# Kernel optimization log

Measured on AMD Instinct MI355X. Metric: run time of the kernel, lower is better.

Reference implementation:

```python
import jax, jax.numpy as jnp
import numpy as np

N, N_EMB, HEAD, N_SEG = 8192, 256, 64, 128  # 128 molecules x 64 atoms


def setup_inputs() -> dict:
    key = jax.random.key(0)
    k0, k1, k2, k3, k4, k5 = jax.random.split(key, 6)
    X = jax.random.normal(k0, (N, N_EMB), dtype=jnp.float32)
    Z = jax.random.normal(k1, (N, 3), dtype=jnp.float32) * 3.0  # coordinates (Angstrom-ish)
    # CSR segment boundaries: 128 equal molecules of 64 atoms
    ptr = jnp.arange(N_SEG + 1, dtype=jnp.int32) * (N // N_SEG)
    scale = 1.0 / np.sqrt(N_EMB)
    Wk = jax.random.normal(k2, (HEAD, N_EMB), dtype=jnp.float32) * scale
    Wq = jax.random.normal(k3, (HEAD, N_EMB), dtype=jnp.float32) * scale
    Wv = jax.random.normal(k4, (HEAD, N_EMB), dtype=jnp.float32) * scale
    # invr0 = (rand(1) + 0.5) / cutoff, cutoff = 4.0
    invr0 = (jax.random.uniform(k5, (1,), dtype=jnp.float32) + 0.5) / 4.0
    return {"X": X, "Z": Z, "Wk": Wk, "Wq": Wq, "Wv": Wv, "invr0": invr0, "ptr": ptr}


def reference(X, Z, Wk, Wq, Wv, invr0, ptr):
    head_size = Wk.shape[0]
    n = X.shape[0]
    K = X @ Wk.T  # [N, H]
    Q = X @ Wq.T  # [N, H]
    V = X @ Wv.T  # [N, H]
    wei = (Q @ K.T) * (head_size ** -0.5)  # [N, N]
    # block-diagonal mask from segment boundaries (== torch.block_diag of ones blocks)
    seg = jnp.searchsorted(ptr[1:], jnp.arange(n, dtype=ptr.dtype), side="right")
    mask = seg[:, None] == seg[None, :]
    wei = jnp.where(mask, wei, -jnp.inf)
    wei = jax.nn.softmax(wei, axis=-1)
    # Euclidean cdist via gram trick, safe sqrt (zero grad at d2<=0, like torch.cdist)
    z2 = jnp.sum(Z * Z, axis=-1)
    d2 = jnp.maximum(z2[:, None] + z2[None, :] - 2.0 * (Z @ Z.T), 0.0)
    dist = jnp.sqrt(jnp.where(d2 > 0, d2, 1.0)) * (d2 > 0)
    wei = wei * jnp.exp(-invr0[0] * dist)
    out = wei @ V  # [N, H]
    return out
```

## Files before the change

### kernel.cpp

```cpp
#include <hip/hip_runtime.h>

#define NATOMS 8192
#define EMB    256
#define HEAD   64
#define WP     264
#define PB     72

typedef _Float16 f16;
typedef f16   f16x8 __attribute__((ext_vector_type(8)));
typedef f16   f16x4 __attribute__((ext_vector_type(4)));
typedef float f32x4 __attribute__((ext_vector_type(4)));

__global__ __launch_bounds__(512) void fused_kernel(
    const float* __restrict__ X, const float* __restrict__ Z,
    const float* __restrict__ Wk, const float* __restrict__ Wq,
    const float* __restrict__ Wv, const float* __restrict__ invr0p,
    float* __restrict__ out)
{
  union __align__(16) SMem {
    struct {
      f16 Xs[64 * WP];
      f16 Ws[192 * WP];
    } a;
    struct {
      f16 Qb[32 * PB];
      f16 Kb[64 * PB];
      f16 Vt[64 * PB];
      f16 Pb[32 * PB];
      float2 part[4][32];
      float zx[64], zy[64], zz[64];
    } b;
  };
  __shared__ SMem sm;

  const int tid  = threadIdx.x;
  const int seg  = blockIdx.x >> 1;
  const int hf   = blockIdx.x & 1;
  const int base = seg * 64;

  const int wave = tid >> 6;
  const int lane = tid & 63;
  const int fr   = lane & 15;
  const int fq   = lane >> 4;
  const int mf0  = (wave >> 2) * 2;
  const int nf0  = (wave & 3) * 3;

  const float ir = invr0p[0];
  float zr0 = 0.f, zr1 = 0.f, zr2 = 0.f;
  if (tid < 64) {
    const float* zp = Z + (size_t)(base + tid) * 3;
    zr0 = zp[0]; zr1 = zp[1]; zr2 = zp[2];
  }

  float4 xv[8];
  #pragma unroll
  for (int i = 0; i < 8; ++i) {
    const int f = tid + i * 512;
    const int row = f >> 6, c4 = f & 63;
    xv[i] = *reinterpret_cast<const float4*>(
        X + (size_t)(base + row) * EMB + c4 * 4);
  }
  float4 wv1[12];
  #pragma unroll
  for (int i = 0; i < 12; ++i) {
    const int f = tid + i * 512;
    const int row = f >> 6, c4 = f & 63;
    const float* src = (row < 64) ? (Wq + (size_t)row * EMB)
                                  : (Wk + (size_t)(row - 64) * EMB);
    wv1[i] = *reinterpret_cast<const float4*>(src + c4 * 4);
  }
  #pragma unroll
  for (int i = 0; i < 8; ++i) {
    const int f = tid + i * 512;
    const int row = f >> 6, c4 = f & 63;
    f16x4 h = {(f16)xv[i].x, (f16)xv[i].y, (f16)xv[i].z, (f16)xv[i].w};
    *reinterpret_cast<f16x4*>(&sm.a.Xs[row * WP + c4 * 4]) = h;
  }
  float4 wv2[12];
  #pragma unroll
  for (int i = 0; i < 12; ++i) {
    const int f = tid + (12 + i) * 512;
    const int row = f >> 6, c4 = f & 63;
    const float* src = (row < 128) ? (Wk + (size_t)(row - 64) * EMB)
                                   : (Wv + (size_t)(row - 128) * EMB);
    wv2[i] = *reinterpret_cast<const float4*>(src + c4 * 4);
  }
  #pragma unroll
  for (int i = 0; i < 12; ++i) {
    const int f = tid + i * 512;
    const int row = f >> 6, c4 = f & 63;
    f16x4 h = {(f16)wv1[i].x, (f16)wv1[i].y, (f16)wv1[i].z, (f16)wv1[i].w};
    *reinterpret_cast<f16x4*>(&sm.a.Ws[row * WP + c4 * 4]) = h;
  }
  #pragma unroll
  for (int i = 0; i < 12; ++i) {
    const int f = tid + (12 + i) * 512;
    const int row = f >> 6, c4 = f & 63;
    f16x4 h = {(f16)wv2[i].x, (f16)wv2[i].y, (f16)wv2[i].z, (f16)wv2[i].w};
    *reinterpret_cast<f16x4*>(&sm.a.Ws[row * WP + c4 * 4]) = h;
  }
  __syncthreads();

  f32x4 acc[2][3];
  #pragma unroll
  for (int m = 0; m < 2; ++m)
    #pragma unroll
    for (int n = 0; n < 3; ++n) acc[m][n] = (f32x4){0.f, 0.f, 0.f, 0.f};

  #pragma unroll
  for (int c = 0; c < 4; ++c) {
    #pragma unroll
    for (int ks = 0; ks < 2; ++ks) {
      const int ko = c * 64 + ks * 32 + fq * 8;
      const f16x8 a0 = *reinterpret_cast<const f16x8*>(
          &sm.a.Xs[((mf0 + 0) * 16 + fr) * WP + ko]);
      const f16x8 a1 = *reinterpret_cast<const f16x8*>(
          &sm.a.Xs[((mf0 + 1) * 16 + fr) * WP + ko]);
      #pragma unroll
      for (int n = 0; n < 3; ++n) {
        const f16x8 b = *reinterpret_cast<const f16x8*>(
            &sm.a.Ws[((nf0 + n) * 16 + fr) * WP + ko]);
        acc[0][n] = __builtin_amdgcn_mfma_f32_16x16x32_f16(a0, b, acc[0][n], 0, 0, 0);
        acc[1][n] = __builtin_amdgcn_mfma_f32_16x16x32_f16(a1, b, acc[1][n], 0, 0, 0);
      }
    }
  }
  __syncthreads();

  #pragma unroll
  for (int m = 0; m < 2; ++m) {
    const int mf = mf0 + m;
    const int rr = mf * 16 + fq * 4;
    #pragma unroll
    for (int n = 0; n < 3; ++n) {
      const int nf  = nf0 + n;
      const int col = nf * 16 + fr;
      if (nf < 4) {
        if ((mf >> 1) == hf) {
          const int qr = rr & 31;
          #pragma unroll
          for (int j = 0; j < 4; ++j)
            sm.b.Qb[(qr + j) * PB + col] = (f16)(acc[m][n][j] * 0.125f);
        }
      } else if (nf < 8) {
        #pragma unroll
        for (int j = 0; j < 4; ++j)
          sm.b.Kb[(rr + j) * PB + (col - 64)] = (f16)acc[m][n][j];
      } else {
        f16x4 hv = {(f16)acc[m][n][0], (f16)acc[m][n][1],
                    (f16)acc[m][n][2], (f16)acc[m][n][3]};
        *reinterpret_cast<f16x4*>(&sm.b.Vt[(col - 128) * PB + rr]) = hv;
      }
    }
  }
  if (tid < 64) {
    sm.b.zx[tid] = zr0; sm.b.zy[tid] = zr1; sm.b.zz[tid] = zr2;
  }
  __syncthreads();

  const int kf = wave & 3;
  const int qf = wave >> 2;
  f32x4 s = (f32x4){0.f, 0.f, 0.f, 0.f};
  #pragma unroll
  for (int hs = 0; hs < 2; ++hs) {
    const int ho = hs * 32 + fq * 8;
    const f16x8 kfrag = *reinterpret_cast<const f16x8*>(
        &sm.b.Kb[(kf * 16 + fr) * PB + ho]);
    const f16x8 qfrag = *reinterpret_cast<const f16x8*>(
        &sm.b.Qb[(qf * 16 + fr) * PB + ho]);
    s = __builtin_amdgcn_mfma_f32_16x16x32_f16(kfrag, qfrag, s, 0, 0, 0);
  }

  float m16 = fmaxf(fmaxf(s[0], s[1]), fmaxf(s[2], s[3]));
  m16 = fmaxf(m16, __shfl_xor(m16, 16));
  m16 = fmaxf(m16, __shfl_xor(m16, 32));
  float e[4]; float s16 = 0.f;
  #pragma unroll
  for (int j = 0; j < 4; ++j) { e[j] = __expf(s[j] - m16); s16 += e[j]; }
  s16 += __shfl_xor(s16, 16);
  s16 += __shfl_xor(s16, 32);
  if (fq == 0) sm.b.part[kf][qf * 16 + fr] = make_float2(m16, s16);
  __syncthreads();

  const float2 p0 = sm.b.part[0][qf * 16 + fr];
  const float2 p1 = sm.b.part[1][qf * 16 + fr];
  const float2 p2 = sm.b.part[2][qf * 16 + fr];
  const float2 p3 = sm.b.part[3][qf * 16 + fr];
  const float mg = fmaxf(fmaxf(p0.x, p1.x), fmaxf(p2.x, p3.x));
  const float sum = p0.y * __expf(p0.x - mg) + p1.y * __expf(p1.x - mg)
                  + p2.y * __expf(p2.x - mg) + p3.y * __expf(p3.x - mg);
  const float myscale = __expf(m16 - mg) / sum;

  const int   ri = hf * 32 + qf * 16 + fr;
  const float rx = sm.b.zx[ri], ry = sm.b.zy[ri], rz = sm.b.zz[ri];
  f16x4 pv;
  #pragma unroll
  for (int j = 0; j < 4; ++j) {
    const int ka = kf * 16 + fq * 4 + j;
    const float dx = rx - sm.b.zx[ka];
    const float dy = ry - sm.b.zy[ka];
    const float dz = rz - sm.b.zz[ka];
    const float dist = sqrtf(dx * dx + dy * dy + dz * dz);
    pv[j] = (f16)(e[j] * myscale * __expf(-ir * dist));
  }
  *reinterpret_cast<f16x4*>(
      &sm.b.Pb[(qf * 16 + fr) * PB + kf * 16 + fq * 4]) = pv;
  __syncthreads();

  const int qf2 = wave & 1;
  const int hb  = wave >> 1;
  f32x4 o = (f32x4){0.f, 0.f, 0.f, 0.f};
  #pragma unroll
  for (int ks2 = 0; ks2 < 2; ++ks2) {
    const int ko2 = ks2 * 32 + fq * 8;
    const f16x8 pf = *reinterpret_cast<const f16x8*>(
        &sm.b.Pb[(qf2 * 16 + fr) * PB + ko2]);
    const f16x8 vf = *reinterpret_cast<const f16x8*>(
        &sm.b.Vt[(hb * 16 + fr) * PB + ko2]);
    o = __builtin_amdgcn_mfma_f32_16x16x32_f16(pf, vf, o, 0, 0, 0);
  }
  #pragma unroll
  for (int j = 0; j < 4; ++j)
    out[(size_t)(base + hf * 32 + qf2 * 16 + fq * 4 + j) * HEAD
        + hb * 16 + fr] = o[j];
}

extern "C" void kernel_launch(void* const* d_in, const int* in_sizes, int n_in,
                              void* d_out, int out_size, void* d_ws, size_t ws_size,
                              hipStream_t stream) {
  const float* X     = (const float*)d_in[0];
  const float* Z     = (const float*)d_in[1];
  const float* Wk    = (const float*)d_in[2];
  const float* Wq    = (const float*)d_in[3];
  const float* Wv    = (const float*)d_in[4];
  const float* invr0 = (const float*)d_in[5];

  fused_kernel<<<dim3(NATOMS / 32), dim3(512), 0, stream>>>(
      X, Z, Wk, Wq, Wv, invr0, (float*)d_out);
}
```

Baseline: 12.05 us.

## Keep weights in registers, split each molecule across four blocks of 16 queries

Weights are no longer staged in shared memory. Each wave streams its own 16 rows of Wk/Wv (plus Wq for the first four waves) straight into registers as MFMA B-fragments, software-pipelined one chunk ahead. This removes the large weight LDS tile and its barrier, and shrinks LDS so more blocks fit per CU (launch bounds now allow 4). The grid doubles to 16-query blocks with a swizzled block index. Each block recomputes the full K and V projection for its molecule, so redundant projection work and X/weight reads grow, and half the waves sit idle in the later phases.

```diff
diff --git a/kernel.cpp b/kernel.cpp
--- a/kernel.cpp
+++ b/kernel.cpp
@@ -3,7 +3,7 @@
 #define NATOMS 8192
 #define EMB    256
 #define HEAD   64
-#define WP     264
+#define XP     264
 #define PB     72
 
 typedef _Float16 f16;
@@ -11,39 +11,41 @@
 typedef f16   f16x4 __attribute__((ext_vector_type(4)));
 typedef float f32x4 __attribute__((ext_vector_type(4)));
 
-__global__ __launch_bounds__(512) void fused_kernel(
+__device__ __forceinline__ f16x8 cvt8(float4 a, float4 b) {
+  return (f16x8){(f16)a.x, (f16)a.y, (f16)a.z, (f16)a.w,
+                 (f16)b.x, (f16)b.y, (f16)b.z, (f16)b.w};
+}
+
+__global__ __launch_bounds__(512, 4) void fused_kernel(
     const float* __restrict__ X, const float* __restrict__ Z,
     const float* __restrict__ Wk, const float* __restrict__ Wq,
     const float* __restrict__ Wv, const float* __restrict__ invr0p,
     float* __restrict__ out)
 {
   union __align__(16) SMem {
+    f16 Xs[64 * XP];
     struct {
-      f16 Xs[64 * WP];
-      f16 Ws[192 * WP];
-    } a;
-    struct {
-      f16 Qb[32 * PB];
+      f16 Qb[16 * PB];
       f16 Kb[64 * PB];
       f16 Vt[64 * PB];
-      f16 Pb[32 * PB];
-      float2 part[4][32];
+      f16 Pb[16 * PB];
+      float2 part[4][16];
       float zx[64], zy[64], zz[64];
     } b;
   };
   __shared__ SMem sm;
 
-  const int tid  = threadIdx.x;
-  const int seg  = blockIdx.x >> 1;
-  const int hf   = blockIdx.x & 1;
-  const int base = seg * 64;
+  const int tid   = threadIdx.x;
+  const int wid   = (blockIdx.x & 7) * 64 + (blockIdx.x >> 3);
+  const int seg   = wid >> 2;
+  const int quad  = wid & 3;
+  const int base  = seg * 64;
+  const int qrow0 = base + quad * 16;
 
   const int wave = tid >> 6;
   const int lane = tid & 63;
   const int fr   = lane & 15;
   const int fq   = lane >> 4;
-  const int mf0  = (wave >> 2) * 2;
-  const int nf0  = (wave & 3) * 3;
 
   const float ir = invr0p[0];
   float zr0 = 0.f, zr1 = 0.f, zr2 = 0.f;
@@ -52,105 +54,96 @@
     zr0 = zp[0]; zr1 = zp[1]; zr2 = zp[2];
   }
 
+  const float* wkv = (wave < 4)
+      ? (Wk + (size_t)(wave * 16 + fr) * EMB)
+      : (Wv + (size_t)((wave - 4) * 16 + fr) * EMB);
+  const float* wqp = Wq + (size_t)((wave & 3) * 16 + fr) * EMB;
+  const bool hasQ = (wave < 4);
+
+#define WLOAD(c, r) do {                                               \
+    const float* _p = wkv + (c) * 64 + fq * 8;                         \
+    r[0] = *reinterpret_cast<const float4*>(_p);                       \
+    r[1] = *reinterpret_cast<const float4*>(_p + 4);                   \
+    r[2] = *reinterpret_cast<const float4*>(_p + 32);                  \
+    r[3] = *reinterpret_cast<const float4*>(_p + 36);                  \
+    if (hasQ) {                                                        \
+      const float* _q = wqp + (c) * 64 + fq * 8;                       \
+      r[4] = *reinterpret_cast<const float4*>(_q);                     \
+      r[5] = *reinterpret_cast<const float4*>(_q + 4);                 \
+      r[6] = *reinterpret_cast<const float4*>(_q + 32);                \
+      r[7] = *reinterpret_cast<const float4*>(_q + 36);                \
+    }                                                                  \
+  } while (0)
+
   float4 xv[8];
   #pragma unroll
   for (int i = 0; i < 8; ++i) {
     const int f = tid + i * 512;
-    const int row = f >> 6, c4 = f & 63;
     xv[i] = *reinterpret_cast<const float4*>(
-        X + (size_t)(base + row) * EMB + c4 * 4);
-  }
-  float4 wv1[12];
-  #pragma unroll
-  for (int i = 0; i < 12; ++i) {
-    const int f = tid + i * 512;
-    const int row = f >> 6, c4 = f & 63;
-    const float* src = (row < 64) ? (Wq + (size_t)row * EMB)
-                                  : (Wk + (size_t)(row - 64) * EMB);
-    wv1[i] = *reinterpret_cast<const float4*>(src + c4 * 4);
-  }
+        X + (size_t)(base + (f >> 6)) * EMB + (f & 63) * 4);
+  }
+  float4 cw[8];
+  WLOAD(0, cw);
   #pragma unroll
   for (int i = 0; i < 8; ++i) {
     const int f = tid + i * 512;
-    const int row = f >> 6, c4 = f & 63;
     f16x4 h = {(f16)xv[i].x, (f16)xv[i].y, (f16)xv[i].z, (f16)xv[i].w};
-    *reinterpret_cast<f16x4*>(&sm.a.Xs[row * WP + c4 * 4]) = h;
-  }
-  float4 wv2[12];
-  #pragma unroll
-  for (int i = 0; i < 12; ++i) {
-    const int f = tid + (12 + i) * 512;
-    const int row = f >> 6, c4 = f & 63;
-    const float* src = (row < 128) ? (Wk + (size_t)(row - 64) * EMB)
-                                   : (Wv + (size_t)(row - 128) * EMB);
-    wv2[i] = *reinterpret_cast<const float4*>(src + c4 * 4);
-  }
-  #pragma unroll
-  for (int i = 0; i < 12; ++i) {
-    const int f = tid + i * 512;
-    const int row = f >> 6, c4 = f & 63;
-    f16x4 h = {(f16)wv1[i].x, (f16)wv1[i].y, (f16)wv1[i].z, (f16)wv1[i].w};
-    *reinterpret_cast<f16x4*>(&sm.a.Ws[row * WP + c4 * 4]) = h;
-  }
-  #pragma unroll
-  for (int i = 0; i < 12; ++i) {
-    const int f = tid + (12 + i) * 512;
-    const int row = f >> 6, c4 = f & 63;
-    f16x4 h = {(f16)wv2[i].x, (f16)wv2[i].y, (f16)wv2[i].z, (f16)wv2[i].w};
-    *reinterpret_cast<f16x4*>(&sm.a.Ws[row * WP + c4 * 4]) = h;
-  }
-  __syncthreads();
-
-  f32x4 acc[2][3];
-  #pragma unroll
-  for (int m = 0; m < 2; ++m)
-    #pragma unroll
-    for (int n = 0; n < 3; ++n) acc[m][n] = (f32x4){0.f, 0.f, 0.f, 0.f};
+    *reinterpret_cast<f16x4*>(&sm.Xs[(f >> 6) * XP + (f & 63) * 4]) = h;
+  }
+  __syncthreads();
+
+  f32x4 akv[4];
+  f32x4 aq = (f32x4){0.f, 0.f, 0.f, 0.f};
+  #pragma unroll
+  for (int mf = 0; mf < 4; ++mf) akv[mf] = (f32x4){0.f, 0.f, 0.f, 0.f};
 
   #pragma unroll
   for (int c = 0; c < 4; ++c) {
+    float4 nw[8];
+    if (c < 3) WLOAD(c + 1, nw);
+    f16x8 bkv[2], bq[2];
+    bkv[0] = cvt8(cw[0], cw[1]);
+    bkv[1] = cvt8(cw[2], cw[3]);
+    if (hasQ) { bq[0] = cvt8(cw[4], cw[5]); bq[1] = cvt8(cw[6], cw[7]); }
     #pragma unroll
     for (int ks = 0; ks < 2; ++ks) {
       const int ko = c * 64 + ks * 32 + fq * 8;
-      const f16x8 a0 = *reinterpret_cast<const f16x8*>(
-          &sm.a.Xs[((mf0 + 0) * 16 + fr) * WP + ko]);
-      const f16x8 a1 = *reinterpret_cast<const f16x8*>(
-          &sm.a.Xs[((mf0 + 1) * 16 + fr) * WP + ko]);
-      #pragma unroll
-      for (int n = 0; n < 3; ++n) {
-        const f16x8 b = *reinterpret_cast<const f16x8*>(
-            &sm.a.Ws[((nf0 + n) * 16 + fr) * WP + ko]);
-        acc[0][n] = __builtin_amdgcn_mfma_f32_16x16x32_f16(a0, b, acc[0][n], 0, 0, 0);
-        acc[1][n] = __builtin_amdgcn_mfma_f32_16x16x32_f16(a1, b, acc[1][n], 0, 0, 0);
+      f16x8 a[4];
+      #pragma unroll
+      for (int mf = 0; mf < 4; ++mf)
+        a[mf] = *reinterpret_cast<const f16x8*>(&sm.Xs[(mf * 16 + fr) * XP + ko]);
+      #pragma unroll
+      for (int mf = 0; mf < 4; ++mf)
+        akv[mf] = __builtin_amdgcn_mfma_f32_16x16x32_f16(a[mf], bkv[ks], akv[mf], 0, 0, 0);
+      if (hasQ) {
+        const f16x8 aqf = *reinterpret_cast<const f16x8*>(
+            &sm.Xs[(quad * 16 + fr) * XP + ko]);
+        aq = __builtin_amdgcn_mfma_f32_16x16x32_f16(aqf, bq[ks], aq, 0, 0, 0);
       }
     }
-  }
-  __syncthreads();
-
-  #pragma unroll
-  for (int m = 0; m < 2; ++m) {
-    const int mf = mf0 + m;
-    const int rr = mf * 16 + fq * 4;
-    #pragma unroll
-    for (int n = 0; n < 3; ++n) {
-      const int nf  = nf0 + n;
-      const int col = nf * 16 + fr;
-      if (nf < 4) {
-        if ((mf >> 1) == hf) {
-          const int qr = rr & 31;
-          #pragma unroll
-          for (int j = 0; j < 4; ++j)
-            sm.b.Qb[(qr + j) * PB + col] = (f16)(acc[m][n][j] * 0.125f);
-        }
-      } else if (nf < 8) {
-        #pragma unroll
-        for (int j = 0; j < 4; ++j)
-          sm.b.Kb[(rr + j) * PB + (col - 64)] = (f16)acc[m][n][j];
-      } else {
-        f16x4 hv = {(f16)acc[m][n][0], (f16)acc[m][n][1],
-                    (f16)acc[m][n][2], (f16)acc[m][n][3]};
-        *reinterpret_cast<f16x4*>(&sm.b.Vt[(col - 128) * PB + rr]) = hv;
-      }
+    if (c < 3) {
+      #pragma unroll
+      for (int i = 0; i < 8; ++i) cw[i] = nw[i];
+    }
+  }
+  __syncthreads();
+
+  if (hasQ) {
+    #pragma unroll
+    for (int j = 0; j < 4; ++j)
+      sm.b.Qb[(fq * 4 + j) * PB + wave * 16 + fr] = (f16)(aq[j] * 0.125f);
+    #pragma unroll
+    for (int mf = 0; mf < 4; ++mf)
+      #pragma unroll
+      for (int j = 0; j < 4; ++j)
+        sm.b.Kb[(mf * 16 + fq * 4 + j) * PB + wave * 16 + fr] = (f16)akv[mf][j];
+  } else {
+    #pragma unroll
+    for (int mf = 0; mf < 4; ++mf) {
+      f16x4 hv = {(f16)akv[mf][0], (f16)akv[mf][1],
+                  (f16)akv[mf][2], (f16)akv[mf][3]};
+      *reinterpret_cast<f16x4*>(
+          &sm.b.Vt[((wave - 4) * 16 + fr) * PB + mf * 16 + fq * 4]) = hv;
     }
   }
   if (tid < 64) {
@@ -158,71 +151,72 @@
   }
   __syncthreads();
 
-  const int kf = wave & 3;
-  const int qf = wave >> 2;
-  f32x4 s = (f32x4){0.f, 0.f, 0.f, 0.f};
-  #pragma unroll
-  for (int hs = 0; hs < 2; ++hs) {
-    const int ho = hs * 32 + fq * 8;
-    const f16x8 kfrag = *reinterpret_cast<const f16x8*>(
-        &sm.b.Kb[(kf * 16 + fr) * PB + ho]);
-    const f16x8 qfrag = *reinterpret_cast<const f16x8*>(
-        &sm.b.Qb[(qf * 16 + fr) * PB + ho]);
-    s = __builtin_amdgcn_mfma_f32_16x16x32_f16(kfrag, qfrag, s, 0, 0, 0);
-  }
-
-  float m16 = fmaxf(fmaxf(s[0], s[1]), fmaxf(s[2], s[3]));
-  m16 = fmaxf(m16, __shfl_xor(m16, 16));
-  m16 = fmaxf(m16, __shfl_xor(m16, 32));
-  float e[4]; float s16 = 0.f;
-  #pragma unroll
-  for (int j = 0; j < 4; ++j) { e[j] = __expf(s[j] - m16); s16 += e[j]; }
-  s16 += __shfl_xor(s16, 16);
-  s16 += __shfl_xor(s16, 32);
-  if (fq == 0) sm.b.part[kf][qf * 16 + fr] = make_float2(m16, s16);
-  __syncthreads();
-
-  const float2 p0 = sm.b.part[0][qf * 16 + fr];
-  const float2 p1 = sm.b.part[1][qf * 16 + fr];
-  const float2 p2 = sm.b.part[2][qf * 16 + fr];
-  const float2 p3 = sm.b.part[3][qf * 16 + fr];
-  const float mg = fmaxf(fmaxf(p0.x, p1.x), fmaxf(p2.x, p3.x));
-  const float sum = p0.y * __expf(p0.x - mg) + p1.y * __expf(p1.x - mg)
-                  + p2.y * __expf(p2.x - mg) + p3.y * __expf(p3.x - mg);
-  const float myscale = __expf(m16 - mg) / sum;
-
-  const int   ri = hf * 32 + qf * 16 + fr;
-  const float rx = sm.b.zx[ri], ry = sm.b.zy[ri], rz = sm.b.zz[ri];
-  f16x4 pv;
-  #pragma unroll
-  for (int j = 0; j < 4; ++j) {
-    const int ka = kf * 16 + fq * 4 + j;
-    const float dx = rx - sm.b.zx[ka];
-    const float dy = ry - sm.b.zy[ka];
-    const float dz = rz - sm.b.zz[ka];
-    const float dist = sqrtf(dx * dx + dy * dy + dz * dz);
-    pv[j] = (f16)(e[j] * myscale * __expf(-ir * dist));
-  }
-  *reinterpret_cast<f16x4*>(
-      &sm.b.Pb[(qf * 16 + fr) * PB + kf * 16 + fq * 4]) = pv;
-  __syncthreads();
-
-  const int qf2 = wave & 1;
-  const int hb  = wave >> 1;
-  f32x4 o = (f32x4){0.f, 0.f, 0.f, 0.f};
-  #pragma unroll
-  for (int ks2 = 0; ks2 < 2; ++ks2) {
-    const int ko2 = ks2 * 32 + fq * 8;
-    const f16x8 pf = *reinterpret_cast<const f16x8*>(
-        &sm.b.Pb[(qf2 * 16 + fr) * PB + ko2]);
-    const f16x8 vf = *reinterpret_cast<const f16x8*>(
-        &sm.b.Vt[(hb * 16 + fr) * PB + ko2]);
-    o = __builtin_amdgcn_mfma_f32_16x16x32_f16(pf, vf, o, 0, 0, 0);
-  }
-  #pragma unroll
-  for (int j = 0; j < 4; ++j)
-    out[(size_t)(base + hf * 32 + qf2 * 16 + fq * 4 + j) * HEAD
-        + hb * 16 + fr] = o[j];
+  float e[4], m16 = -1e30f;
+  if (wave < 4) {
+    const int kf = wave;
+    f32x4 s = (f32x4){0.f, 0.f, 0.f, 0.f};
+    #pragma unroll
+    for (int hs = 0; hs < 2; ++hs) {
+      const int ho = hs * 32 + fq * 8;
+      const f16x8 kfrag = *reinterpret_cast<const f16x8*>(
+          &sm.b.Kb[(kf * 16 + fr) * PB + ho]);
+      const f16x8 qfrag = *reinterpret_cast<const f16x8*>(
+          &sm.b.Qb[fr * PB + ho]);
+      s = __builtin_amdgcn_mfma_f32_16x16x32_f16(kfrag, qfrag, s, 0, 0, 0);
+    }
+    m16 = fmaxf(fmaxf(s[0], s[1]), fmaxf(s[2], s[3]));
+    m16 = fmaxf(m16, __shfl_xor(m16, 16));
+    m16 = fmaxf(m16, __shfl_xor(m16, 32));
+    float s16 = 0.f;
+    #pragma unroll
+    for (int j = 0; j < 4; ++j) { e[j] = __expf(s[j] - m16); s16 += e[j]; }
+    s16 += __shfl_xor(s16, 16);
+    s16 += __shfl_xor(s16, 32);
+    if (fq == 0) sm.b.part[kf][fr] = make_float2(m16, s16);
+  }
+  __syncthreads();
+
+  if (wave < 4) {
+    const float2 p0 = sm.b.part[0][fr];
+    const float2 p1 = sm.b.part[1][fr];
+    const float2 p2 = sm.b.part[2][fr];
+    const float2 p3 = sm.b.part[3][fr];
+    const float mg = fmaxf(fmaxf(p0.x, p1.x), fmaxf(p2.x, p3.x));
+    const float sum = p0.y * __expf(p0.x - mg) + p1.y * __expf(p1.x - mg)
+                    + p2.y * __expf(p2.x - mg) + p3.y * __expf(p3.x - mg);
+    const float myscale = __expf(m16 - mg) / sum;
+    const int   ri = quad * 16 + fr;
+    const float rx = sm.b.zx[ri], ry = sm.b.zy[ri], rz = sm.b.zz[ri];
+    f16x4 pv;
+    #pragma unroll
+    for (int j = 0; j < 4; ++j) {
+      const int ka = wave * 16 + fq * 4 + j;
+      const float dx = rx - sm.b.zx[ka];
+      const float dy = ry - sm.b.zy[ka];
+      const float dz = rz - sm.b.zz[ka];
+      const float dist = sqrtf(dx * dx + dy * dy + dz * dz);
+      pv[j] = (f16)(e[j] * myscale * __expf(-ir * dist));
+    }
+    *reinterpret_cast<f16x4*>(&sm.b.Pb[fr * PB + wave * 16 + fq * 4]) = pv;
+  }
+  __syncthreads();
+
+  if (wave >= 4) {
+    const int hb = wave - 4;
+    f32x4 o = (f32x4){0.f, 0.f, 0.f, 0.f};
+    #pragma unroll
+    for (int ks2 = 0; ks2 < 2; ++ks2) {
+      const int ko2 = ks2 * 32 + fq * 8;
+      const f16x8 pf = *reinterpret_cast<const f16x8*>(&sm.b.Pb[fr * PB + ko2]);
+      const f16x8 vf = *reinterpret_cast<const f16x8*>(
+          &sm.b.Vt[(hb * 16 + fr) * PB + ko2]);
+      o = __builtin_amdgcn_mfma_f32_16x16x32_f16(pf, vf, o, 0, 0, 0);
+    }
+    #pragma unroll
+    for (int j = 0; j < 4; ++j)
+      out[(size_t)(qrow0 + fq * 4 + j) * HEAD + hb * 16 + fr] = o[j];
+  }
+#undef WLOAD
 }
 
 extern "C" void kernel_launch(void* const* d_in, const int* in_sizes, int n_in,
@@ -235,6 +229,6 @@
   const float* Wv    = (const float*)d_in[4];
   const float* invr0 = (const float*)d_in[5];
 
-  fused_kernel<<<dim3(NATOMS / 32), dim3(512), 0, stream>>>(
+  fused_kernel<<<dim3(NATOMS / 16), dim3(512), 0, stream>>>(
       X, Z, Wk, Wq, Wv, invr0, (float*)d_out);
 }
```

New measurement: 19.81 us. 1.64x slower.

## Split X load into two halves overlapped with projection MFMAs and remap blocks across XCDs

Applied to the files above, without the earlier changes.

X is now loaded in two column halves. The second half is fetched from global memory after the first sync, while the MFMAs over the first half of the embedding run, then written to LDS behind an extra barrier. Block indices are also remapped so that the two halves of a segment land on blocks with the same blockIdx&7, which likely groups them on one XCD for L2 sharing of X. The cost is an extra __syncthreads and more live registers.

```diff
diff --git a/kernel.cpp b/kernel.cpp
--- a/kernel.cpp
+++ b/kernel.cpp
@@ -3,7 +3,7 @@
 #define NATOMS 8192
 #define EMB    256
 #define HEAD   64
-#define WP     264
+#define XP     264
 #define PB     72
 
 typedef _Float16 f16;
@@ -19,8 +19,8 @@
 {
   union __align__(16) SMem {
     struct {
-      f16 Xs[64 * WP];
-      f16 Ws[192 * WP];
+      f16 Xs[64 * XP];
+      f16 Ws[192 * XP];
     } a;
     struct {
       f16 Qb[32 * PB];
@@ -34,8 +34,9 @@
   __shared__ SMem sm;
 
   const int tid  = threadIdx.x;
-  const int seg  = blockIdx.x >> 1;
-  const int hf   = blockIdx.x & 1;
+  const int wid  = (blockIdx.x & 7) * 32 + (blockIdx.x >> 3);
+  const int seg  = wid >> 1;
+  const int hf   = wid & 1;
   const int base = seg * 64;
 
   const int wave = tid >> 6;
@@ -52,12 +53,12 @@
     zr0 = zp[0]; zr1 = zp[1]; zr2 = zp[2];
   }
 
-  float4 xv[8];
-  #pragma unroll
-  for (int i = 0; i < 8; ++i) {
-    const int f = tid + i * 512;
-    const int row = f >> 6, c4 = f & 63;
-    xv[i] = *reinterpret_cast<const float4*>(
+  float4 xv0[4];
+  #pragma unroll
+  for (int i = 0; i < 4; ++i) {
+    const int u = tid + i * 512;
+    const int row = u >> 5, c4 = u & 31;
+    xv0[i] = *reinterpret_cast<const float4*>(
         X + (size_t)(base + row) * EMB + c4 * 4);
   }
   float4 wv1[12];
@@ -69,13 +70,6 @@
                                   : (Wk + (size_t)(row - 64) * EMB);
     wv1[i] = *reinterpret_cast<const float4*>(src + c4 * 4);
   }
-  #pragma unroll
-  for (int i = 0; i < 8; ++i) {
-    const int f = tid + i * 512;
-    const int row = f >> 6, c4 = f & 63;
-    f16x4 h = {(f16)xv[i].x, (f16)xv[i].y, (f16)xv[i].z, (f16)xv[i].w};
-    *reinterpret_cast<f16x4*>(&sm.a.Xs[row * WP + c4 * 4]) = h;
-  }
   float4 wv2[12];
   #pragma unroll
   for (int i = 0; i < 12; ++i) {
@@ -85,21 +79,38 @@
                                    : (Wv + (size_t)(row - 128) * EMB);
     wv2[i] = *reinterpret_cast<const float4*>(src + c4 * 4);
   }
+
+  #pragma unroll
+  for (int i = 0; i < 4; ++i) {
+    const int u = tid + i * 512;
+    const int row = u >> 5, c4 = u & 31;
+    f16x4 h = {(f16)xv0[i].x, (f16)xv0[i].y, (f16)xv0[i].z, (f16)xv0[i].w};
+    *reinterpret_cast<f16x4*>(&sm.a.Xs[row * XP + c4 * 4]) = h;
+  }
   #pragma unroll
   for (int i = 0; i < 12; ++i) {
     const int f = tid + i * 512;
     const int row = f >> 6, c4 = f & 63;
     f16x4 h = {(f16)wv1[i].x, (f16)wv1[i].y, (f16)wv1[i].z, (f16)wv1[i].w};
-    *reinterpret_cast<f16x4*>(&sm.a.Ws[row * WP + c4 * 4]) = h;
+    *reinterpret_cast<f16x4*>(&sm.a.Ws[row * XP + c4 * 4]) = h;
   }
   #pragma unroll
   for (int i = 0; i < 12; ++i) {
     const int f = tid + (12 + i) * 512;
     const int row = f >> 6, c4 = f & 63;
     f16x4 h = {(f16)wv2[i].x, (f16)wv2[i].y, (f16)wv2[i].z, (f16)wv2[i].w};
-    *reinterpret_cast<f16x4*>(&sm.a.Ws[row * WP + c4 * 4]) = h;
-  }
-  __syncthreads();
+    *reinterpret_cast<f16x4*>(&sm.a.Ws[row * XP + c4 * 4]) = h;
+  }
+  __syncthreads();
+
+  float4 xv1[4];
+  #pragma unroll
+  for (int i = 0; i < 4; ++i) {
+    const int u = tid + i * 512;
+    const int row = u >> 5, c4 = (u & 31) + 32;
+    xv1[i] = *reinterpret_cast<const float4*>(
+        X + (size_t)(base + row) * EMB + c4 * 4);
+  }
 
   f32x4 acc[2][3];
   #pragma unroll
@@ -108,18 +119,46 @@
     for (int n = 0; n < 3; ++n) acc[m][n] = (f32x4){0.f, 0.f, 0.f, 0.f};
 
   #pragma unroll
-  for (int c = 0; c < 4; ++c) {
+  for (int c = 0; c < 2; ++c) {
     #pragma unroll
     for (int ks = 0; ks < 2; ++ks) {
       const int ko = c * 64 + ks * 32 + fq * 8;
       const f16x8 a0 = *reinterpret_cast<const f16x8*>(
-          &sm.a.Xs[((mf0 + 0) * 16 + fr) * WP + ko]);
+          &sm.a.Xs[((mf0 + 0) * 16 + fr) * XP + ko]);
       const f16x8 a1 = *reinterpret_cast<const f16x8*>(
-          &sm.a.Xs[((mf0 + 1) * 16 + fr) * WP + ko]);
+          &sm.a.Xs[((mf0 + 1) * 16 + fr) * XP + ko]);
       #pragma unroll
       for (int n = 0; n < 3; ++n) {
         const f16x8 b = *reinterpret_cast<const f16x8*>(
-            &sm.a.Ws[((nf0 + n) * 16 + fr) * WP + ko]);
+            &sm.a.Ws[((nf0 + n) * 16 + fr) * XP + ko]);
+        acc[0][n] = __builtin_amdgcn_mfma_f32_16x16x32_f16(a0, b, acc[0][n], 0, 0, 0);
+        acc[1][n] = __builtin_amdgcn_mfma_f32_16x16x32_f16(a1, b, acc[1][n], 0, 0, 0);
+      }
+    }
+  }
+
+  #pragma unroll
+  for (int i = 0; i < 4; ++i) {
+    const int u = tid + i * 512;
+    const int row = u >> 5, c4 = (u & 31) + 32;
+    f16x4 h = {(f16)xv1[i].x, (f16)xv1[i].y, (f16)xv1[i].z, (f16)xv1[i].w};
+    *reinterpret_cast<f16x4*>(&sm.a.Xs[row * XP + c4 * 4]) = h;
+  }
+  __syncthreads();
+
+  #pragma unroll
+  for (int c = 2; c < 4; ++c) {
+    #pragma unroll
+    for (int ks = 0; ks < 2; ++ks) {
+      const int ko = c * 64 + ks * 32 + fq * 8;
+      const f16x8 a0 = *reinterpret_cast<const f16x8*>(
+          &sm.a.Xs[((mf0 + 0) * 16 + fr) * XP + ko]);
+      const f16x8 a1 = *reinterpret_cast<const f16x8*>(
+          &sm.a.Xs[((mf0 + 1) * 16 + fr) * XP + ko]);
+      #pragma unroll
+      for (int n = 0; n < 3; ++n) {
+        const f16x8 b = *reinterpret_cast<const f16x8*>(
+            &sm.a.Ws[((nf0 + n) * 16 + fr) * XP + ko]);
         acc[0][n] = __builtin_amdgcn_mfma_f32_16x16x32_f16(a0, b, acc[0][n], 0, 0, 0);
         acc[1][n] = __builtin_amdgcn_mfma_f32_16x16x32_f16(a1, b, acc[1][n], 0, 0, 0);
       }
```

Measured after the change: 12.17 us. Within noise of the previous version (+1.0%).
